# Kernel tuning notes

Measured on AMD Instinct MI355X. Metric: run time of the kernel, lower is better.

The kernel has to match this reference:

```python
import jax, jax.numpy as jnp
import numpy as np

VOC, TOPIC, EMB, BATCH = 128000, 512, 1024, 1024

def setup_inputs() -> dict:
    key = jax.random.key(0)
    k1, k2, k3 = jax.random.split(key, 3)
    x = jax.random.normal(k1, (TOPIC, BATCH), dtype=jnp.float32)
    beta0 = jax.random.normal(k2, (VOC, EMB), dtype=jnp.float32)
    beta_t = jax.random.normal(k3, (TOPIC, EMB), dtype=jnp.float32) * 0.02  # nn.init.normal_(std=0.02)
    return {"x": x, "beta0": beta0, "beta_t": beta_t, "t": 0}

def reference(x, beta0, beta_t, t):
    # w: [voc, topic] = beta0 [voc, emb] @ beta_t.T [emb, topic]
    # (the t==0 branch and else branch are identical in the source)
    w = jnp.einsum('ve,te->vt', beta0, beta_t)
    w = jax.nn.softmax(w, axis=0)  # softmax over vocab dim (dim=0)
    # out: [voc, batch]
    return jnp.einsum('vt,tb->vb', w, x)
```

## Files before the change

### kernel.cpp

```cpp
#include <hip/hip_runtime.h>

typedef _Float16 f16x8 __attribute__((ext_vector_type(8)));
typedef float    f32x4 __attribute__((ext_vector_type(4)));
typedef unsigned short u16;

#define VOC   128000
#define TOPIC 512
#define EMB   1024
#define BATCH 1024
#define ROWB  128

__device__ __forceinline__ int swz(int row, int kbyte) {
    return row * ROWB + (kbyte ^ ((row & 7) << 4));
}
__device__ __forceinline__ int xcd_swz(int bid, int nwg) {
    int x = bid & 7, o = bid >> 3, q = nwg >> 3, r = nwg & 7;
    return (x < r ? x * (q + 1) : r * (q + 1) + (x - r) * q) + o;
}
union H2U { _Float16 h; u16 u; };

#define SBAR() asm volatile("s_barrier" ::: "memory")
#define WVM0() asm volatile("s_waitcnt vmcnt(0)" ::: "memory")
#define WLG0() asm volatile("s_waitcnt lgkmcnt(0)" ::: "memory")

#define GLDS(SRC, DST) __builtin_amdgcn_global_load_lds( \
    (const __attribute__((address_space(1))) unsigned int*)(SRC), \
    (__attribute__((address_space(3))) unsigned int*)(DST), 16, 0, 0)

#define RD_A(MH, KS) { _Pragma("unroll") \
    for (int m = 0; m < 4; ++m) \
        af[m] = *(const f16x8*)(bufA + wr * 16384 + \
            swz((MH) * 64 + m * 16 + lr, (KS) * 64 + lk * 16)); }
#define RD_B(KS) { _Pragma("unroll") \
    for (int n = 0; n < 4; ++n) \
        bf[n] = *(const f16x8*)(bufB + (wc >> 1) * 16384 + \
            swz((wc & 1) * 64 + n * 16 + lr, (KS) * 64 + lk * 16)); }
#define MFMA16(MH) { \
    __builtin_amdgcn_s_setprio(1); \
    _Pragma("unroll") for (int m = 0; m < 4; ++m) \
    _Pragma("unroll") for (int n = 0; n < 4; ++n) \
        acc[(MH) * 4 + m][n] = __builtin_amdgcn_mfma_f32_16x16x32_f16( \
            af[m], bf[n], acc[(MH) * 4 + m][n], 0, 0, 0); \
    __builtin_amdgcn_s_setprio(0); }

__global__ void cvt_betat_kernel(const float* __restrict__ betat, u16* __restrict__ bt16) {
    const size_t g = (size_t)blockIdx.x * 256 + threadIdx.x;
    const float4* src = reinterpret_cast<const float4*>(betat) + g * 2;
    float4 a = src[0], b = src[1];
    f16x8 h;
    h[0]=(_Float16)a.x; h[1]=(_Float16)a.y; h[2]=(_Float16)a.z; h[3]=(_Float16)a.w;
    h[4]=(_Float16)b.x; h[5]=(_Float16)b.y; h[6]=(_Float16)b.z; h[7]=(_Float16)b.w;
    *(reinterpret_cast<f16x8*>(bt16) + g) = h;
}

__global__ __launch_bounds__(512, 2) void gemm1_kernel(
    const float* __restrict__ beta0, const u16* __restrict__ bt16,
    u16* __restrict__ Eg, float* __restrict__ sg)
{
    __shared__ char lds[131072];

    const int tid  = threadIdx.x;
    const int lane = tid & 63;
    const int wid  = tid >> 6;
    const int wr = wid >> 2, wc = wid & 3;
    const int lr = lane & 15, lk = lane >> 4;
    const int srow8  = lane >> 3;
    const int schunk = ((lane & 7) ^ srow8) * 8;

    const int bid   = xcd_swz(blockIdx.x, gridDim.x);
    const int tile  = bid >> 1;
    const int chunk = bid & 1;
    const int v0 = tile * 256, t0 = chunk * 256;

    const int a_row = tid >> 1, a_kh = tid & 1;
    const float* aRowP = beta0 + (size_t)(v0 + a_row) * EMB + a_kh * 32;

    f32x4 acc[8][4] = {};
    f16x8 af[4], bf[4];
    float4 rA[8];

    auto loadA4 = [&](int kt, int j0) {
        const float4* g = reinterpret_cast<const float4*>(aRowP + kt * 64);
        #pragma unroll
        for (int j = 0; j < 4; ++j) rA[j0 + j] = g[j0 + j];
    };
    auto cvtA = [&](int kt1, int j0) {
        char* dA = lds + (kt1 & 1) * 65536 + (a_row >> 7) * 16384;
        const int rl = a_row & 127;
        #pragma unroll
        for (int jj = 0; jj < 2; ++jj) {
            float4 xx = rA[j0 + jj * 2], yy = rA[j0 + jj * 2 + 1];
            f16x8 h;
            h[0]=(_Float16)xx.x; h[1]=(_Float16)xx.y; h[2]=(_Float16)xx.z; h[3]=(_Float16)xx.w;
            h[4]=(_Float16)yy.x; h[5]=(_Float16)yy.y; h[6]=(_Float16)yy.z; h[7]=(_Float16)yy.w;
            *(f16x8*)(dA + swz(rl, (a_kh * 4 + (j0 >> 1) + jj) * 16)) = h;
        }
    };
    auto stageB = [&](int kt, int h) {
        char* dstb = lds + (kt & 1) * 65536 + 32768 + h * 16384;
        #pragma unroll
        for (int q = 0; q < 2; ++q) {
            const u16* s_ = bt16 + (size_t)(t0 + h * 128 + wid * 16 + q * 8 + srow8) * EMB
                          + kt * 64 + schunk;
            GLDS(s_, dstb + (wid * 16 + q * 8) * ROWB);
        }
    };

    loadA4(0, 0); loadA4(0, 4);
    stageB(0, 0); stageB(0, 1);
    cvtA(0, 0); cvtA(0, 4);
    WLG0();

    for (int t = 0; t < 16; ++t) {
        char* bufA = lds + (t & 1) * 65536;
        char* bufB = bufA + 32768;
        const bool st = (t + 1) < 16;

        WVM0();
        SBAR();
        RD_A(0, 0); RD_B(0);
        if (st) { loadA4(t + 1, 0); stageB(t + 1, 0); }
        MFMA16(0);
        SBAR();
        RD_A(1, 0);
        if (st) { loadA4(t + 1, 4); stageB(t + 1, 1); }
        MFMA16(1);
        SBAR();
        RD_A(0, 1); RD_B(1);
        if (st) cvtA(t + 1, 0);
        MFMA16(0);
        SBAR();
        RD_A(1, 1);
        if (st) cvtA(t + 1, 4);
        MFMA16(1);
        WLG0();
    }

    __syncthreads();
    u16* ldsE = reinterpret_cast<u16*>(lds);
    float csum = 0.f;
    #pragma unroll
    for (int c = 0; c < 4; ++c) {
        if (wr == (c >> 1)) {
            const int mb = (c & 1) * 4;
            #pragma unroll
            for (int m = 0; m < 4; ++m)
              #pragma unroll
              for (int n = 0; n < 4; ++n)
                #pragma unroll
                for (int r = 0; r < 4; ++r) {
                    const int row = m * 16 + lk * 4 + r;
                    const int col = wc * 64 + n * 16 + lr;
                    H2U cv; cv.h = (_Float16)__expf(acc[mb + m][n][r]);
                    ldsE[row * 264 + col] = cv.u;
                }
        }
        __syncthreads();
        {
            const int row8 = tid >> 3, seg = tid & 7;
            const int4* sp = reinterpret_cast<const int4*>(&ldsE[row8 * 264 + seg * 32]);
            u16* dst = Eg + (size_t)(v0 + c * 64 + row8) * 2048 + t0 + seg * 32;
            int4 a0 = sp[0], a1 = sp[1], a2 = sp[2], a3 = sp[3];
            int4* dp = reinterpret_cast<int4*>(dst);
            dp[0] = a0; dp[1] = a1; dp[2] = a2; dp[3] = a3;
        }
        if (tid < 256) {
            float s = 0.f;
            for (int r = 0; r < 64; ++r) { H2U cv; cv.u = ldsE[r * 264 + tid]; s += (float)cv.h; }
            csum += s;
        }
        __syncthreads();
    }
    if (tid < 256) atomicAdd(sg + t0 + tid, csum);
}

__global__ void xst_kernel(const float* __restrict__ x, const float* __restrict__ s,
                           u16* __restrict__ xsT)
{
    __shared__ float tile[32][33];
    const int b0 = blockIdx.x * 32, t0 = blockIdx.y * 32;
    const int tx = threadIdx.x, ty = threadIdx.y;
    tile[ty][tx] = x[(size_t)(t0 + ty) * BATCH + b0 + tx];
    __syncthreads();
    const float sc = 65536.0f / s[t0 + tx];
    H2U cv; cv.h = (_Float16)(tile[tx][ty] * sc);
    xsT[(size_t)(b0 + ty) * TOPIC + t0 + tx] = cv.u;
}

__global__ __launch_bounds__(512, 2) void gemm2_kernel(
    const u16* __restrict__ Eg, const u16* __restrict__ xsT,
    float* __restrict__ out, int c0, int nch)
{
    __shared__ char lds[131072];

    const int tid  = threadIdx.x;
    const int lane = tid & 63;
    const int wid  = tid >> 6;
    const int wr = wid >> 2, wc = wid & 3;
    const int lr = lane & 15, lk = lane >> 4;
    const int srow8  = lane >> 3;
    const int schunk = ((lane & 7) ^ srow8) * 8;

    const int bid   = xcd_swz(blockIdx.x, gridDim.x);
    const int tile  = bid / nch;
    const int chunk = bid % nch;
    const int v0 = tile * 256, b0 = (c0 + chunk) * 256;

    f32x4 acc[8][4] = {};
    f16x8 af[4], bf[4];

    auto stageA = [&](int kt, int h) {
        char* dsta = lds + (kt & 1) * 65536 + h * 16384;
        #pragma unroll
        for (int q = 0; q < 2; ++q) {
            const u16* s_ = Eg + (size_t)(v0 + h * 128 + wid * 16 + q * 8 + srow8) * 2048
                          + kt * 64 + schunk;
            GLDS(s_, dsta + (wid * 16 + q * 8) * ROWB);
        }
    };
    auto stageB = [&](int kt, int h) {
        char* dstb = lds + (kt & 1) * 65536 + 32768 + h * 16384;
        #pragma unroll
        for (int q = 0; q < 2; ++q) {
            const u16* s_ = xsT + (size_t)(b0 + h * 128 + wid * 16 + q * 8 + srow8) * TOPIC
                          + kt * 64 + schunk;
            GLDS(s_, dstb + (wid * 16 + q * 8) * ROWB);
        }
    };

    stageA(0, 0); stageA(0, 1); stageB(0, 0); stageB(0, 1);

    for (int t = 0; t < 8; ++t) {
        char* bufA = lds + (t & 1) * 65536;
        char* bufB = bufA + 32768;
        const bool st = (t + 1) < 8;

        WVM0();
        SBAR();
        RD_A(0, 0); RD_B(0);
        if (st) stageA(t + 1, 0);
        MFMA16(0);
        SBAR();
        RD_A(1, 0);
        if (st) stageA(t + 1, 1);
        MFMA16(1);
        SBAR();
        RD_A(0, 1); RD_B(1);
        if (st) stageB(t + 1, 0);
        MFMA16(0);
        SBAR();
        RD_A(1, 1);
        if (st) stageB(t + 1, 1);
        MFMA16(1);
    }

    #pragma unroll
    for (int mh = 0; mh < 2; ++mh)
      #pragma unroll
      for (int m = 0; m < 4; ++m)
        #pragma unroll
        for (int n = 0; n < 4; ++n)
          #pragma unroll
          for (int r = 0; r < 4; ++r) {
              const int row = wr * 128 + mh * 64 + m * 16 + lk * 4 + r;
              const int col = wc * 64 + n * 16 + lr;
              out[(size_t)(v0 + row) * BATCH + b0 + col] = acc[mh * 4 + m][n][r] * 0x1p-16f;
          }
}

extern "C" void kernel_launch(void* const* d_in, const int* in_sizes, int n_in,
                              void* d_out, int out_size, void* d_ws, size_t ws_size,
                              hipStream_t stream)
{
    const float* x     = (const float*)d_in[0];
    const float* beta0 = (const float*)d_in[1];
    const float* betat = (const float*)d_in[2];
    float* out = (float*)d_out;

    const size_t need_min = 4096 + (size_t)BATCH * TOPIC * 2;
    if (ws_size < need_min) return;
    float* s_g  = (float*)d_ws;
    u16*   buf1 = (u16*)((char*)d_ws + 4096);

    hipMemsetAsync(d_ws, 0, 2048, stream);
    cvt_betat_kernel<<<256, 256, 0, stream>>>(betat, buf1);

    u16* EgO = (u16*)d_out;
    gemm1_kernel<<<1000, 512, 0, stream>>>(beta0, buf1, EgO, s_g);

    xst_kernel<<<dim3(BATCH / 32, TOPIC / 32), dim3(32, 32), 0, stream>>>(x, s_g, buf1);

    gemm2_kernel<<<1500, 512, 0, stream>>>(EgO, buf1, out, 1, 3);
    gemm2_kernel<<<500,  512, 0, stream>>>(EgO, buf1, out, 0, 1);
}
```

Before: 569.5 us.

## Deepen GEMM pipelines to 4-stage K=32 ring buffers with partial vmcnt waits

Both GEMM kernels change from double-buffered K=64 tiles to a four-slot ring of K=32 tiles, prefetching three tiles ahead and waiting on vmcnt(8) instead of vmcnt(0). This lets global loads stay in flight across iterations and hides latency better. The LDS swizzle is changed to 64-byte rows. In gemm1 the fp32 beta0 register loads are double-buffered two tiles ahead, and conversion happens one tile ahead. The cost is more barriers per unit of K, a smaller MFMA batch between barriers, and fragile hand-counted vmcnt values.

```diff
diff --git a/kernel.cpp b/kernel.cpp
--- a/kernel.cpp
+++ b/kernel.cpp
@@ -8,10 +8,9 @@
 #define TOPIC 512
 #define EMB   1024
 #define BATCH 1024
-#define ROWB  128
-
-__device__ __forceinline__ int swz(int row, int kbyte) {
-    return row * ROWB + (kbyte ^ ((row & 7) << 4));
+
+__device__ __forceinline__ int swz32(int row, int kbyte) {
+    return row * 64 + (kbyte ^ (((row >> 1) & 3) << 4));
 }
 __device__ __forceinline__ int xcd_swz(int bid, int nwg) {
     int x = bid & 7, o = bid >> 3, q = nwg >> 3, r = nwg & 7;
@@ -21,20 +20,20 @@
 
 #define SBAR() asm volatile("s_barrier" ::: "memory")
 #define WVM0() asm volatile("s_waitcnt vmcnt(0)" ::: "memory")
+#define WVM4() asm volatile("s_waitcnt vmcnt(4)" ::: "memory")
+#define WVM8() asm volatile("s_waitcnt vmcnt(8)" ::: "memory")
 #define WLG0() asm volatile("s_waitcnt lgkmcnt(0)" ::: "memory")
 
 #define GLDS(SRC, DST) __builtin_amdgcn_global_load_lds( \
     (const __attribute__((address_space(1))) unsigned int*)(SRC), \
     (__attribute__((address_space(3))) unsigned int*)(DST), 16, 0, 0)
 
-#define RD_A(MH, KS) { _Pragma("unroll") \
+#define RD_A(BUF, MH) { _Pragma("unroll") \
     for (int m = 0; m < 4; ++m) \
-        af[m] = *(const f16x8*)(bufA + wr * 16384 + \
-            swz((MH) * 64 + m * 16 + lr, (KS) * 64 + lk * 16)); }
-#define RD_B(KS) { _Pragma("unroll") \
+        af[m] = *(const f16x8*)((BUF) + swz32(wr * 128 + (MH) * 64 + m * 16 + lr, lk * 16)); }
+#define RD_B(BUF) { _Pragma("unroll") \
     for (int n = 0; n < 4; ++n) \
-        bf[n] = *(const f16x8*)(bufB + (wc >> 1) * 16384 + \
-            swz((wc & 1) * 64 + n * 16 + lr, (KS) * 64 + lk * 16)); }
+        bf[n] = *(const f16x8*)((BUF) + 16384 + swz32(wc * 64 + n * 16 + lr, lk * 16)); }
 #define MFMA16(MH) { \
     __builtin_amdgcn_s_setprio(1); \
     _Pragma("unroll") for (int m = 0; m < 4; ++m) \
@@ -64,76 +63,63 @@
     const int wid  = tid >> 6;
     const int wr = wid >> 2, wc = wid & 3;
     const int lr = lane & 15, lk = lane >> 4;
-    const int srow8  = lane >> 3;
-    const int schunk = ((lane & 7) ^ srow8) * 8;
+    const int srcRow   = lane >> 2;
+    const int srcChunk = (lane & 3) ^ ((lane >> 3) & 3);
 
     const int bid   = xcd_swz(blockIdx.x, gridDim.x);
     const int tile  = bid >> 1;
     const int chunk = bid & 1;
     const int v0 = tile * 256, t0 = chunk * 256;
 
-    const int a_row = tid >> 1, a_kh = tid & 1;
-    const float* aRowP = beta0 + (size_t)(v0 + a_row) * EMB + a_kh * 32;
+    const int arow = tid >> 1, ahalf = tid & 1;
+    const float* aBase = beta0 + (size_t)(v0 + arow) * EMB + ahalf * 16;
 
     f32x4 acc[8][4] = {};
     f16x8 af[4], bf[4];
-    float4 rA[8];
-
-    auto loadA4 = [&](int kt, int j0) {
-        const float4* g = reinterpret_cast<const float4*>(aRowP + kt * 64);
-        #pragma unroll
-        for (int j = 0; j < 4; ++j) rA[j0 + j] = g[j0 + j];
+    float4 rEv[4], rOd[4];
+
+#define G1_LOADA(R, KT) { const float4* gp = (const float4*)(aBase + (KT) * 32); \
+    R[0] = gp[0]; R[1] = gp[1]; R[2] = gp[2]; R[3] = gp[3]; }
+#define G1_CVT(R, KT1) { char* dA = lds + ((KT1) & 3) * 32768; \
+    f16x8 h0, h1; \
+    h0[0]=(_Float16)R[0].x; h0[1]=(_Float16)R[0].y; h0[2]=(_Float16)R[0].z; h0[3]=(_Float16)R[0].w; \
+    h0[4]=(_Float16)R[1].x; h0[5]=(_Float16)R[1].y; h0[6]=(_Float16)R[1].z; h0[7]=(_Float16)R[1].w; \
+    h1[0]=(_Float16)R[2].x; h1[1]=(_Float16)R[2].y; h1[2]=(_Float16)R[2].z; h1[3]=(_Float16)R[2].w; \
+    h1[4]=(_Float16)R[3].x; h1[5]=(_Float16)R[3].y; h1[6]=(_Float16)R[3].z; h1[7]=(_Float16)R[3].w; \
+    *(f16x8*)(dA + swz32(arow, (ahalf * 2) * 16)) = h0; \
+    *(f16x8*)(dA + swz32(arow, (ahalf * 2 + 1) * 16)) = h1; }
+
+    auto stageB_ = [&](int kt) {
+        char* dst = lds + (kt & 3) * 32768 + 16384;
+        const u16* s0 = bt16 + (size_t)(t0 + wid * 32 + srcRow) * EMB + kt * 32 + srcChunk * 8;
+        GLDS(s0, dst + wid * 32 * 64);
+        GLDS(s0 + (size_t)16 * EMB, dst + (wid * 32 + 16) * 64);
     };
-    auto cvtA = [&](int kt1, int j0) {
-        char* dA = lds + (kt1 & 1) * 65536 + (a_row >> 7) * 16384;
-        const int rl = a_row & 127;
-        #pragma unroll
-        for (int jj = 0; jj < 2; ++jj) {
-            float4 xx = rA[j0 + jj * 2], yy = rA[j0 + jj * 2 + 1];
-            f16x8 h;
-            h[0]=(_Float16)xx.x; h[1]=(_Float16)xx.y; h[2]=(_Float16)xx.z; h[3]=(_Float16)xx.w;
-            h[4]=(_Float16)yy.x; h[5]=(_Float16)yy.y; h[6]=(_Float16)yy.z; h[7]=(_Float16)yy.w;
-            *(f16x8*)(dA + swz(rl, (a_kh * 4 + (j0 >> 1) + jj) * 16)) = h;
-        }
-    };
-    auto stageB = [&](int kt, int h) {
-        char* dstb = lds + (kt & 1) * 65536 + 32768 + h * 16384;
-        #pragma unroll
-        for (int q = 0; q < 2; ++q) {
-            const u16* s_ = bt16 + (size_t)(t0 + h * 128 + wid * 16 + q * 8 + srow8) * EMB
-                          + kt * 64 + schunk;
-            GLDS(s_, dstb + (wid * 16 + q * 8) * ROWB);
-        }
-    };
-
-    loadA4(0, 0); loadA4(0, 4);
-    stageB(0, 0); stageB(0, 1);
-    cvtA(0, 0); cvtA(0, 4);
+
+    stageB_(0);
+    G1_LOADA(rEv, 0);
+    stageB_(1); stageB_(2);
+    G1_LOADA(rOd, 1);
+    G1_CVT(rEv, 0);
     WLG0();
 
-    for (int t = 0; t < 16; ++t) {
-        char* bufA = lds + (t & 1) * 65536;
-        char* bufB = bufA + 32768;
-        const bool st = (t + 1) < 16;
-
-        WVM0();
-        SBAR();
-        RD_A(0, 0); RD_B(0);
-        if (st) { loadA4(t + 1, 0); stageB(t + 1, 0); }
-        MFMA16(0);
-        SBAR();
-        RD_A(1, 0);
-        if (st) { loadA4(t + 1, 4); stageB(t + 1, 1); }
-        MFMA16(1);
-        SBAR();
-        RD_A(0, 1); RD_B(1);
-        if (st) cvtA(t + 1, 0);
-        MFMA16(0);
-        SBAR();
-        RD_A(1, 1);
-        if (st) cvtA(t + 1, 4);
-        MFMA16(1);
-        WLG0();
+#define G1_TILE(T, RC, RI) { \
+    WVM8(); SBAR(); \
+    char* buf = lds + ((T) & 3) * 32768; \
+    RD_A(buf, 0); RD_B(buf); \
+    if ((T) + 2 < 32) G1_LOADA(RI, (T) + 2); \
+    MFMA16(0); \
+    SBAR(); \
+    RD_A(buf, 1); \
+    if ((T) + 1 < 32) G1_CVT(RC, (T) + 1); \
+    if ((T) + 3 < 32) stageB_((T) + 3); \
+    MFMA16(1); \
+    WLG0(); }
+
+    for (int tt = 0; tt < 16; ++tt) {
+        const int t = tt * 2;
+        G1_TILE(t,     rOd, rEv);
+        G1_TILE(t + 1, rEv, rOd);
     }
 
     __syncthreads();
@@ -198,8 +184,8 @@
     const int wid  = tid >> 6;
     const int wr = wid >> 2, wc = wid & 3;
     const int lr = lane & 15, lk = lane >> 4;
-    const int srow8  = lane >> 3;
-    const int schunk = ((lane & 7) ^ srow8) * 8;
+    const int srcRow   = lane >> 2;
+    const int srcChunk = (lane & 3) ^ ((lane >> 3) & 3);
 
     const int bid   = xcd_swz(blockIdx.x, gridDim.x);
     const int tile  = bid / nch;
@@ -209,48 +195,31 @@
     f32x4 acc[8][4] = {};
     f16x8 af[4], bf[4];
 
-    auto stageA = [&](int kt, int h) {
-        char* dsta = lds + (kt & 1) * 65536 + h * 16384;
-        #pragma unroll
-        for (int q = 0; q < 2; ++q) {
-            const u16* s_ = Eg + (size_t)(v0 + h * 128 + wid * 16 + q * 8 + srow8) * 2048
-                          + kt * 64 + schunk;
-            GLDS(s_, dsta + (wid * 16 + q * 8) * ROWB);
-        }
+    auto stageA_ = [&](int kt) {
+        char* dst = lds + (kt & 3) * 32768;
+        const u16* s0 = Eg + (size_t)(v0 + wid * 32 + srcRow) * 2048 + kt * 32 + srcChunk * 8;
+        GLDS(s0, dst + wid * 32 * 64);
+        GLDS(s0 + (size_t)16 * 2048, dst + (wid * 32 + 16) * 64);
     };
-    auto stageB = [&](int kt, int h) {
-        char* dstb = lds + (kt & 1) * 65536 + 32768 + h * 16384;
-        #pragma unroll
-        for (int q = 0; q < 2; ++q) {
-            const u16* s_ = xsT + (size_t)(b0 + h * 128 + wid * 16 + q * 8 + srow8) * TOPIC
-                          + kt * 64 + schunk;
-            GLDS(s_, dstb + (wid * 16 + q * 8) * ROWB);
-        }
+    auto stageB_ = [&](int kt) {
+        char* dst = lds + (kt & 3) * 32768 + 16384;
+        const u16* s0 = xsT + (size_t)(b0 + wid * 32 + srcRow) * TOPIC + kt * 32 + srcChunk * 8;
+        GLDS(s0, dst + wid * 32 * 64);
+        GLDS(s0 + (size_t)16 * TOPIC, dst + (wid * 32 + 16) * 64);
     };
 
-    stageA(0, 0); stageA(0, 1); stageB(0, 0); stageB(0, 1);
-
-    for (int t = 0; t < 8; ++t) {
-        char* bufA = lds + (t & 1) * 65536;
-        char* bufB = bufA + 32768;
-        const bool st = (t + 1) < 8;
-
-        WVM0();
+    stageA_(0); stageB_(0); stageA_(1); stageB_(1); stageA_(2); stageB_(2);
+
+    for (int t = 0; t < 16; ++t) {
+        if (t <= 13) { WVM8(); } else if (t == 14) { WVM4(); } else { WVM0(); }
         SBAR();
-        RD_A(0, 0); RD_B(0);
-        if (st) stageA(t + 1, 0);
+        char* buf = lds + (t & 3) * 32768;
+        RD_A(buf, 0); RD_B(buf);
+        if (t + 3 < 16) stageA_(t + 3);
         MFMA16(0);
         SBAR();
-        RD_A(1, 0);
-        if (st) stageA(t + 1, 1);
-        MFMA16(1);
-        SBAR();
-        RD_A(0, 1); RD_B(1);
-        if (st) stageB(t + 1, 0);
-        MFMA16(0);
-        SBAR();
-        RD_A(1, 1);
-        if (st) stageB(t + 1, 1);
+        RD_A(buf, 1);
+        if (t + 3 < 16) stageB_(t + 3);
         MFMA16(1);
     }
 
```

Result: faster. 506.7 us (-11.0%).

## Restructure GEMM main loops into 4-phase barrier pipeline with register double-buffered A

Applied to the files above, without the earlier changes.

Both GEMM kernels are rewritten around a four-phase inner schedule. Each phase reads A and B fragments for both k-steps, issues the next prefetch, syncs, and then runs a 4x2x2 MFMA block with partial vmcnt waits instead of full drains. In gemm1 the fp32 beta0 loads are double-buffered in registers (even/odd tiles), so global loads run two tiles ahead and the fp16 conversion happens one tile later. LDS staging layouts are changed to match the new fragment ownership, and the occupancy hint of 2 blocks/CU is dropped. The cost is higher register pressure (af[8], 16 float4 prefetch registers), which may reduce occupancy, and more barriers per tile.

```diff
diff --git a/kernel.cpp b/kernel.cpp
--- a/kernel.cpp
+++ b/kernel.cpp
@@ -21,26 +21,30 @@
 
 #define SBAR() asm volatile("s_barrier" ::: "memory")
 #define WVM0() asm volatile("s_waitcnt vmcnt(0)" ::: "memory")
+#define WVM2() asm volatile("s_waitcnt vmcnt(2)" ::: "memory")
+#define WVM8() asm volatile("s_waitcnt vmcnt(8)" ::: "memory")
 #define WLG0() asm volatile("s_waitcnt lgkmcnt(0)" ::: "memory")
 
 #define GLDS(SRC, DST) __builtin_amdgcn_global_load_lds( \
     (const __attribute__((address_space(1))) unsigned int*)(SRC), \
     (__attribute__((address_space(3))) unsigned int*)(DST), 16, 0, 0)
 
-#define RD_A(MH, KS) { _Pragma("unroll") \
-    for (int m = 0; m < 4; ++m) \
-        af[m] = *(const f16x8*)(bufA + wr * 16384 + \
-            swz((MH) * 64 + m * 16 + lr, (KS) * 64 + lk * 16)); }
-#define RD_B(KS) { _Pragma("unroll") \
-    for (int n = 0; n < 4; ++n) \
-        bf[n] = *(const f16x8*)(bufB + (wc >> 1) * 16384 + \
-            swz((wc & 1) * 64 + n * 16 + lr, (KS) * 64 + lk * 16)); }
-#define MFMA16(MH) { \
-    __builtin_amdgcn_s_setprio(1); \
-    _Pragma("unroll") for (int m = 0; m < 4; ++m) \
-    _Pragma("unroll") for (int n = 0; n < 4; ++n) \
-        acc[(MH) * 4 + m][n] = __builtin_amdgcn_mfma_f32_16x16x32_f16( \
-            af[m], bf[n], acc[(MH) * 4 + m][n], 0, 0, 0); \
+#define RD_AF(BUF, MH) { _Pragma("unroll") \
+    for (int m = 0; m < 4; ++m) { _Pragma("unroll") \
+    for (int ks = 0; ks < 2; ++ks) \
+        af[m*2+ks] = *(const f16x8*)((BUF) + \
+            swz(wr*128 + (MH)*64 + m*16 + lr, ks*64 + lk*16)); } }
+#define RD_BF(BUF, NH) { _Pragma("unroll") \
+    for (int n = 0; n < 2; ++n) { _Pragma("unroll") \
+    for (int ks = 0; ks < 2; ++ks) \
+        bf[n*2+ks] = *(const f16x8*)((BUF) + 32768 + \
+            swz(wc*64 + (NH)*32 + n*16 + lr, ks*64 + lk*16)); } }
+#define MM(MH, NH) { __builtin_amdgcn_s_setprio(1); \
+    _Pragma("unroll") for (int m = 0; m < 4; ++m) { \
+    _Pragma("unroll") for (int n = 0; n < 2; ++n) { \
+    _Pragma("unroll") for (int ks = 0; ks < 2; ++ks) \
+        acc[(MH)*4+m][(NH)*2+n] = __builtin_amdgcn_mfma_f32_16x16x32_f16( \
+            af[m*2+ks], bf[n*2+ks], acc[(MH)*4+m][(NH)*2+n], 0, 0, 0); } } \
     __builtin_amdgcn_s_setprio(0); }
 
 __global__ void cvt_betat_kernel(const float* __restrict__ betat, u16* __restrict__ bt16) {
@@ -53,7 +57,7 @@
     *(reinterpret_cast<f16x8*>(bt16) + g) = h;
 }
 
-__global__ __launch_bounds__(512, 2) void gemm1_kernel(
+__global__ __launch_bounds__(512) void gemm1_kernel(
     const float* __restrict__ beta0, const u16* __restrict__ bt16,
     u16* __restrict__ Eg, float* __restrict__ sg)
 {
@@ -72,68 +76,66 @@
     const int chunk = bid & 1;
     const int v0 = tile * 256, t0 = chunk * 256;
 
-    const int a_row = tid >> 1, a_kh = tid & 1;
-    const float* aRowP = beta0 + (size_t)(v0 + a_row) * EMB + a_kh * 32;
+    const int arow = tid >> 1, ahalf = tid & 1;
+    const float* aBase = beta0 + (size_t)(v0 + arow) * EMB + ahalf * 32;
 
     f32x4 acc[8][4] = {};
-    f16x8 af[4], bf[4];
-    float4 rA[8];
-
-    auto loadA4 = [&](int kt, int j0) {
-        const float4* g = reinterpret_cast<const float4*>(aRowP + kt * 64);
-        #pragma unroll
-        for (int j = 0; j < 4; ++j) rA[j0 + j] = g[j0 + j];
+    f16x8 af[8], bf[4];
+    float4 rEv[8], rOd[8];
+
+#define G1_LOADA(R, KT) { const float4* gp = (const float4*)(aBase + (KT) * 64); \
+    _Pragma("unroll") for (int j = 0; j < 8; ++j) R[j] = gp[j]; }
+#define G1_CVT(R, KT1) { char* dA = lds + ((KT1) & 1) * 65536; \
+    _Pragma("unroll") for (int jj = 0; jj < 4; ++jj) { \
+        float4 x = R[jj*2], y = R[jj*2+1]; \
+        f16x8 h; \
+        h[0]=(_Float16)x.x; h[1]=(_Float16)x.y; h[2]=(_Float16)x.z; h[3]=(_Float16)x.w; \
+        h[4]=(_Float16)y.x; h[5]=(_Float16)y.y; h[6]=(_Float16)y.z; h[7]=(_Float16)y.w; \
+        *(f16x8*)(dA + swz(arow, ahalf * 64 + jj * 16)) = h; } }
+
+    auto stageB = [&](int kt, int h) {
+        char* dst = lds + (kt & 1) * 65536 + 32768;
+        #pragma unroll
+        for (int g = 0; g < 2; ++g) {
+            const int rbase = (g * 2 + (wid >> 2)) * 64 + h * 32 + (wid & 3) * 8;
+            GLDS(bt16 + (size_t)(t0 + rbase + srow8) * EMB + kt * 64 + schunk,
+                 dst + rbase * ROWB);
+        }
     };
-    auto cvtA = [&](int kt1, int j0) {
-        char* dA = lds + (kt1 & 1) * 65536 + (a_row >> 7) * 16384;
-        const int rl = a_row & 127;
-        #pragma unroll
-        for (int jj = 0; jj < 2; ++jj) {
-            float4 xx = rA[j0 + jj * 2], yy = rA[j0 + jj * 2 + 1];
-            f16x8 h;
-            h[0]=(_Float16)xx.x; h[1]=(_Float16)xx.y; h[2]=(_Float16)xx.z; h[3]=(_Float16)xx.w;
-            h[4]=(_Float16)yy.x; h[5]=(_Float16)yy.y; h[6]=(_Float16)yy.z; h[7]=(_Float16)yy.w;
-            *(f16x8*)(dA + swz(rl, (a_kh * 4 + (j0 >> 1) + jj) * 16)) = h;
-        }
-    };
-    auto stageB = [&](int kt, int h) {
-        char* dstb = lds + (kt & 1) * 65536 + 32768 + h * 16384;
-        #pragma unroll
-        for (int q = 0; q < 2; ++q) {
-            const u16* s_ = bt16 + (size_t)(t0 + h * 128 + wid * 16 + q * 8 + srow8) * EMB
-                          + kt * 64 + schunk;
-            GLDS(s_, dstb + (wid * 16 + q * 8) * ROWB);
-        }
-    };
-
-    loadA4(0, 0); loadA4(0, 4);
+
     stageB(0, 0); stageB(0, 1);
-    cvtA(0, 0); cvtA(0, 4);
+    G1_LOADA(rEv, 0);
+    G1_CVT(rEv, 0);
     WLG0();
-
-    for (int t = 0; t < 16; ++t) {
-        char* bufA = lds + (t & 1) * 65536;
-        char* bufB = bufA + 32768;
-        const bool st = (t + 1) < 16;
-
-        WVM0();
-        SBAR();
-        RD_A(0, 0); RD_B(0);
-        if (st) { loadA4(t + 1, 0); stageB(t + 1, 0); }
-        MFMA16(0);
-        SBAR();
-        RD_A(1, 0);
-        if (st) { loadA4(t + 1, 4); stageB(t + 1, 1); }
-        MFMA16(1);
-        SBAR();
-        RD_A(0, 1); RD_B(1);
-        if (st) cvtA(t + 1, 0);
-        MFMA16(0);
-        SBAR();
-        RD_A(1, 1);
-        if (st) cvtA(t + 1, 4);
-        MFMA16(1);
-        WLG0();
+    G1_LOADA(rOd, 1);
+    SBAR();
+
+#define G1_TILE(T, RC, RI) { \
+    const bool st = (T) + 1 < 16; \
+    char* buf = lds + ((T) & 1) * 65536; \
+     \
+    RD_AF(buf, 0); RD_BF(buf, 0); \
+    if (st) stageB((T) + 1, 0); \
+    SBAR(); WLG0(); MM(0, 0); SBAR(); \
+     \
+    RD_BF(buf, 1); \
+    if (st) stageB((T) + 1, 1); \
+    SBAR(); WLG0(); MM(0, 1); SBAR(); \
+     \
+    RD_AF(buf, 1); RD_BF(buf, 0); \
+    if (st) G1_CVT(RC, (T) + 1); \
+    SBAR(); WLG0(); MM(1, 0); SBAR(); \
+     \
+    RD_BF(buf, 1); \
+    if ((T) + 2 < 16) G1_LOADA(RI, (T) + 2); \
+    SBAR(); WLG0(); MM(1, 1); \
+    if ((T) + 2 < 16) { WVM8(); } else { WVM0(); } \
+    SBAR(); }
+
+    for (int tt = 0; tt < 8; ++tt) {
+        const int t = tt * 2;
+        G1_TILE(t,     rOd, rEv);
+        G1_TILE(t + 1, rEv, rOd);
     }
 
     __syncthreads();
@@ -187,7 +189,7 @@
     xsT[(size_t)(b0 + ty) * TOPIC + t0 + tx] = cv.u;
 }
 
-__global__ __launch_bounds__(512, 2) void gemm2_kernel(
+__global__ __launch_bounds__(512) void gemm2_kernel(
     const u16* __restrict__ Eg, const u16* __restrict__ xsT,
     float* __restrict__ out, int c0, int nch)
 {
@@ -207,51 +209,50 @@
     const int v0 = tile * 256, b0 = (c0 + chunk) * 256;
 
     f32x4 acc[8][4] = {};
-    f16x8 af[4], bf[4];
+    f16x8 af[8], bf[4];
 
     auto stageA = [&](int kt, int h) {
-        char* dsta = lds + (kt & 1) * 65536 + h * 16384;
-        #pragma unroll
-        for (int q = 0; q < 2; ++q) {
-            const u16* s_ = Eg + (size_t)(v0 + h * 128 + wid * 16 + q * 8 + srow8) * 2048
-                          + kt * 64 + schunk;
-            GLDS(s_, dsta + (wid * 16 + q * 8) * ROWB);
+        char* dst = lds + (kt & 1) * 65536;
+        #pragma unroll
+        for (int g = 0; g < 2; ++g) {
+            const int rbase = h * 128 + g * 64 + wid * 8;
+            GLDS(Eg + (size_t)(v0 + rbase + srow8) * 2048 + kt * 64 + schunk,
+                 dst + rbase * ROWB);
         }
     };
     auto stageB = [&](int kt, int h) {
-        char* dstb = lds + (kt & 1) * 65536 + 32768 + h * 16384;
-        #pragma unroll
-        for (int q = 0; q < 2; ++q) {
-            const u16* s_ = xsT + (size_t)(b0 + h * 128 + wid * 16 + q * 8 + srow8) * TOPIC
-                          + kt * 64 + schunk;
-            GLDS(s_, dstb + (wid * 16 + q * 8) * ROWB);
+        char* dst = lds + (kt & 1) * 65536 + 32768;
+        #pragma unroll
+        for (int g = 0; g < 2; ++g) {
+            const int rbase = (g * 2 + (wid >> 2)) * 64 + h * 32 + (wid & 3) * 8;
+            GLDS(xsT + (size_t)(b0 + rbase + srow8) * TOPIC + kt * 64 + schunk,
+                 dst + rbase * ROWB);
         }
     };
 
     stageA(0, 0); stageA(0, 1); stageB(0, 0); stageB(0, 1);
+    WVM0();
+    SBAR();
 
     for (int t = 0; t < 8; ++t) {
-        char* bufA = lds + (t & 1) * 65536;
-        char* bufB = bufA + 32768;
         const bool st = (t + 1) < 8;
-
-        WVM0();
+        char* buf = lds + (t & 1) * 65536;
+        RD_AF(buf, 0); RD_BF(buf, 0);
+        if (st) stageA(t + 1, 0);
+        SBAR(); WLG0(); MM(0, 0);
+        if (st) { WVM2(); } else { WVM0(); }
         SBAR();
-        RD_A(0, 0); RD_B(0);
-        if (st) stageA(t + 1, 0);
-        MFMA16(0);
+        RD_BF(buf, 1);
+        if (st) stageA(t + 1, 1);
+        SBAR(); WLG0(); MM(0, 1); SBAR();
+        RD_AF(buf, 1); RD_BF(buf, 0);
+        if (st) stageB(t + 1, 0);
+        SBAR(); WLG0(); MM(1, 0); SBAR();
+        RD_BF(buf, 1);
+        if (st) stageB(t + 1, 1);
+        SBAR(); WLG0(); MM(1, 1);
+        if (st) { WVM2(); } else { WVM0(); }
         SBAR();
-        RD_A(1, 0);
-        if (st) stageA(t + 1, 1);
-        MFMA16(1);
-        SBAR();
-        RD_A(0, 1); RD_B(1);
-        if (st) stageB(t + 1, 0);
-        MFMA16(0);
-        SBAR();
-        RD_A(1, 1);
-        if (st) stageB(t + 1, 1);
-        MFMA16(1);
     }
 
     #pragma unroll
```

New measurement: 566.1 us. No clear change (-0.6%).
